# Kernel optimization log

Hardware: AMD Instinct MI355X
Metric: run time of the kernel (lower is better)

The kernel has to match this reference:

```python
import jax, jax.numpy as jnp
import numpy as np
import math

NB_HEADS = 16
NUM_BUCKETS = 32
MAX_DISTANCE = 128


def _rel_bucket(qlen, klen, num_buckets=NUM_BUCKETS, max_distance=MAX_DISTANCE):
    # static (numpy) computation of T5 relative-position buckets, bidirectional
    relpos = np.arange(qlen)[:, None] - np.arange(klen)[None, :]
    n = -relpos
    nb = num_buckets // 2
    ret = (n < 0).astype(np.int64) * nb
    n = np.abs(n)
    max_exact = nb // 2
    is_small = n < max_exact
    val_if_large = max_exact + (
        np.log(np.maximum(n, 1) / max_exact) / math.log(max_distance / max_exact) * (nb - max_exact)
    ).astype(np.int64)
    val_if_large = np.minimum(val_if_large, nb - 1)
    return ret + np.where(is_small, n, val_if_large)


def _layer_normalize(x):
    # faithful to source: mean/biased-std over last dim, NO epsilon, no affine
    m = jnp.mean(x, axis=-1, keepdims=True)
    var = jnp.mean((x - m) ** 2, axis=-1, keepdims=True)
    return (x - m) / jnp.sqrt(var)


def setup_inputs() -> dict:
    key = jax.random.key(0)
    ks = jax.random.split(key, 16)
    B, L, D, F = 4, 1024, 1024, 4096
    s = 0.02
    inp = {
        "x": jax.random.normal(ks[0], (B, L, D), jnp.float32),
        "padding_mask": jnp.ones((B, L), jnp.int32),
        "Wq": jax.random.normal(ks[1], (D, D), jnp.float32) * s,
        "bq": jnp.zeros((D,), jnp.float32),
        "Wk": jax.random.normal(ks[2], (D, D), jnp.float32) * s,
        "bk": jnp.zeros((D,), jnp.float32),
        "Wv": jax.random.normal(ks[3], (D, D), jnp.float32) * s,
        "bv": jnp.zeros((D,), jnp.float32),
        "Wo": jax.random.normal(ks[4], (D, D), jnp.float32) * s,
        "bo": jnp.zeros((D,), jnp.float32),
        "rel_emb": jax.random.normal(ks[5], (NUM_BUCKETS, NB_HEADS), jnp.float32) * s,
        "W1": jax.random.normal(ks[6], (F, D), jnp.float32) * s,
        "b1": jnp.zeros((F,), jnp.float32),
        "W2": jax.random.normal(ks[7], (D, F), jnp.float32) * s,
        "b2": jnp.zeros((D,), jnp.float32),
    }
    return inp


def reference(x, padding_mask, Wq, bq, Wk, bk, Wv, bv, Wo, bo, rel_emb, W1, b1, W2, b2):
    B, L, D = x.shape
    H = NB_HEADS
    dh = D // H

    q = x @ Wq.T + bq
    k = x @ Wk.T + bk
    v = x @ Wv.T + bv

    # NOTE: source does a RAW reshape (B, L, H*dh) -> (B*H, L, dh); reproduce exactly
    qm = q.reshape(B * H, L, dh)
    km = k.reshape(B * H, L, dh)
    vm = v.reshape(B * H, L, dh)

    scores = jnp.einsum("bqd,bkd->bqk", qm, km)  # (B*H, L, L), no 1/sqrt(dh) scaling in source

    # relative position bias: emb[bucket] -> (L, L, H), tile heads B times, permute
    buckets = jnp.asarray(_rel_bucket(L, L))
    pos = rel_emb[buckets]                      # (L, L, H)
    bias = jnp.transpose(jnp.tile(pos, (1, 1, B)), (2, 0, 1))  # (H*B, L, L)
    scores = scores + bias

    # padding mask in log space, tiled exactly like source's repeat+view
    pm = jnp.log(padding_mask.astype(jnp.float32))            # (B, L)
    mask = jnp.tile(pm[:, None, :], (1, L, H)).reshape(-1, L, L)  # (B*H, L, L)
    scores = scores + mask

    p = jax.nn.softmax(scores, axis=-1)  # dropout is identity at p=0 / eval
    att = (p @ vm).reshape(B, L, D)
    att = att @ Wo.T + bo

    att_out = _layer_normalize(att + x)
    ff = jax.nn.relu(att_out @ W1.T + b1) @ W2.T + b2
    ff_out = _layer_normalize(ff + att_out)
    return ff_out
```

## Files before the change

### kernel.cpp

```cpp
#include <hip/hip_runtime.h>
#include <hip/hip_bf16.h>

typedef __hip_bfloat16 bf16;
typedef __attribute__((ext_vector_type(8))) short s8v;
typedef __attribute__((ext_vector_type(4))) float f32x4;

__device__ __forceinline__ float bits2f(unsigned short u) {
    return __uint_as_float(((unsigned)u) << 16);
}
__device__ __forceinline__ unsigned short f2b(float f) {
    union { float f; unsigned u; } x{f};
    return (unsigned short)((x.u + 0x7fff + ((x.u >> 16) & 1)) >> 16);
}
__device__ __forceinline__ float to_f(float x) { return x; }
__device__ __forceinline__ float to_f(unsigned short x) { return bits2f(x); }

__device__ __forceinline__ void load4(const float* p, float* a) {
    float4 t = *(const float4*)p;
    a[0] = t.x; a[1] = t.y; a[2] = t.z; a[3] = t.w;
}
__device__ __forceinline__ void load4(const unsigned short* p, float* a) {
    ushort4 t = *(const ushort4*)p;
    a[0] = bits2f(t.x); a[1] = bits2f(t.y); a[2] = bits2f(t.z); a[3] = bits2f(t.w);
}

__global__ __launch_bounds__(256)
void cvt_all_kernel(const float* __restrict__ x,
                    const float* __restrict__ Wq, const float* __restrict__ Wk,
                    const float* __restrict__ Wv, const float* __restrict__ Wo,
                    const float* __restrict__ W1, const float* __restrict__ W2,
                    unsigned short* __restrict__ xb, unsigned short* __restrict__ Wqkvb,
                    unsigned short* __restrict__ Wob,
                    unsigned short* __restrict__ W1b, unsigned short* __restrict__ W2b)
{
    int i = blockIdx.x * 256 + threadIdx.x;
    const float* src; unsigned short* dst; int off;
    if (i < (1 << 20))      { src = x;  dst = xb;  off = i; }
    else if (i < (2 << 20)) { src = W1; dst = W1b; off = i - (1 << 20); }
    else if (i < (3 << 20)) { src = W2; dst = W2b; off = i - (2 << 20); }
    else {
        int j = i - (3 << 20);
        int sel = j >> 18;
        off = j & ((1 << 18) - 1);
        src = sel == 0 ? Wq : sel == 1 ? Wk : sel == 2 ? Wv : Wo;
        dst = sel == 3 ? Wob : Wqkvb + ((size_t)sel << 20);
    }
    float4 v = ((const float4*)src)[off];
    ushort4 o = { f2b(v.x), f2b(v.y), f2b(v.z), f2b(v.w) };
    ((ushort4*)dst)[off] = o;
}

__global__ void rbias_kernel(const float* __restrict__ rel_emb, unsigned short* __restrict__ rbias)
{
    int idx = blockIdx.x * 256 + threadIdx.x;
    if (idx >= 16 * 2048) return;
    int h = idx >> 11, q = idx & 2047;
    int n = q - 1023, ret = 0;
    if (n < 0) { ret = 16; n = -n; }
    int b;
    if (n < 8) b = n;
    else {
        double t = log((double)n / 8.0) / log(16.0) * 8.0;
        int v = 8 + (int)t;
        b = v < 15 ? v : 15;
    }
    rbias[idx] = f2b(rel_emb[(ret + b) * 16 + h]);
}

template<typename TC, typename TR, int RELU, int QKV>
__global__ __launch_bounds__(256)
void mfma_gemm(const unsigned short* __restrict__ A, int lda,
               const unsigned short* __restrict__ W, int ldw,
               const float* __restrict__ b0, const float* __restrict__ b1,
               const float* __restrict__ b2,
               const TR* __restrict__ res,
               void* __restrict__ C0, void* __restrict__ C1, void* __restrict__ C2,
               int ldc, int M, int N, int Ksplit)
{
    __shared__ unsigned short sm[4 * 128 * 32];
    const int tid = threadIdx.x;
    const int w = tid >> 6, lane = tid & 63;
    const int quad = lane >> 4, col = lane & 15;

    const int bid = blockIdx.x + gridDim.x * blockIdx.y;
    const int nwg = gridDim.x * gridDim.y;
    const int swz = (bid & 7) * (nwg >> 3) + (bid >> 3);
    const int m0 = (swz / gridDim.x) * 128;
    const int n0 = (swz % gridDim.x) * 128;

    const int wrow = (w & 1) * 64, wcol = (w >> 1) * 64;
    const int kz = blockIdx.z * Ksplit;
    const int NT = Ksplit >> 5;

    int sr0, sq0, sr1, sq1;
    {
        const int i0_ = tid;
        int sp = i0_ & 63, rl = ((sp >> 2) ^ (sp >> 4)) & 1;
        sr0 = ((i0_ >> 6) << 4) | ((sp >> 2) & 0xE) | rl;
        sq0 = (sp & 3) ^ ((((sp >> 3) & 1) << 1) | rl);
        const int i1_ = 256 + tid;
        sp = i1_ & 63; rl = ((sp >> 2) ^ (sp >> 4)) & 1;
        sr1 = ((i1_ >> 6) << 4) | ((sp >> 2) & 0xE) | rl;
        sq1 = (sp & 3) ^ ((((sp >> 3) & 1) << 1) | rl);
    }
    const unsigned off0 = (unsigned)__builtin_amdgcn_readfirstlane((unsigned)((0 * 256 + (tid & 192)) * 16));
    const unsigned off1 = (unsigned)__builtin_amdgcn_readfirstlane((unsigned)((1 * 256 + (tid & 192)) * 16));

#define STAGE32(buf, k0)                                                                     \
    {                                                                                        \
        unsigned short* As_ = sm + (buf) * 4096;                                             \
        unsigned short* Ws_ = sm + 8192 + (buf) * 4096;                                      \
        const unsigned short* ga0 = A + (size_t)(m0 + sr0) * lda + (k0) + sq0 * 8;           \
        __builtin_amdgcn_global_load_lds(                                                    \
            (const __attribute__((address_space(1))) unsigned int*)ga0,                      \
            (__attribute__((address_space(3))) unsigned int*)((char*)As_ + off0), 16, 0, 0); \
        const unsigned short* ga1 = A + (size_t)(m0 + sr1) * lda + (k0) + sq1 * 8;           \
        __builtin_amdgcn_global_load_lds(                                                    \
            (const __attribute__((address_space(1))) unsigned int*)ga1,                      \
            (__attribute__((address_space(3))) unsigned int*)((char*)As_ + off1), 16, 0, 0); \
        const unsigned short* gw0 = W + (size_t)(n0 + sr0) * ldw + (k0) + sq0 * 8;           \
        __builtin_amdgcn_global_load_lds(                                                    \
            (const __attribute__((address_space(1))) unsigned int*)gw0,                      \
            (__attribute__((address_space(3))) unsigned int*)((char*)Ws_ + off0), 16, 0, 0); \
        const unsigned short* gw1 = W + (size_t)(n0 + sr1) * ldw + (k0) + sq1 * 8;           \
        __builtin_amdgcn_global_load_lds(                                                    \
            (const __attribute__((address_space(1))) unsigned int*)gw1,                      \
            (__attribute__((address_space(3))) unsigned int*)((char*)Ws_ + off1), 16, 0, 0); \
    }

    f32x4 acc[4][4] = {};

    STAGE32(0, kz);

    for (int t = 0; t < NT; ++t) {
        __syncthreads();
        const int cur = t & 1;
        if (t + 1 < NT) STAGE32(cur ^ 1, kz + (t + 1) * 32);

        const unsigned short* As = sm + cur * 4096;
        const unsigned short* Ws = sm + 8192 + cur * 4096;
        s8v af[4], bfr[4];
        #pragma unroll
        for (int mt = 0; mt < 4; ++mt) {
            int rr = wrow + mt * 16 + col;
            af[mt] = *(const s8v*)(As + ((rr * 32 + ((quad ^ (rr & 3)) << 3)) ^ (((rr >> 2) & 1) << 5)));
        }
        #pragma unroll
        for (int nt = 0; nt < 4; ++nt) {
            int rr = wcol + nt * 16 + col;
            bfr[nt] = *(const s8v*)(Ws + ((rr * 32 + ((quad ^ (rr & 3)) << 3)) ^ (((rr >> 2) & 1) << 5)));
        }
        __builtin_amdgcn_s_setprio(1);
        #pragma unroll
        for (int mt = 0; mt < 4; ++mt)
            #pragma unroll
            for (int nt = 0; nt < 4; ++nt)
                acc[mt][nt] = __builtin_amdgcn_mfma_f32_16x16x32_bf16(af[mt], bfr[nt], acc[mt][nt], 0, 0, 0);
        __builtin_amdgcn_s_setprio(0);
    }
#undef STAGE32

    if (QKV) {
        const int sel = n0 >> 10;
        unsigned short* Cb = (unsigned short*)(sel == 0 ? C0 : sel == 1 ? C1 : C2);
        const float* bs = sel == 0 ? b0 : sel == 1 ? b1 : b2;
        #pragma unroll
        for (int mt = 0; mt < 4; ++mt)
            #pragma unroll
            for (int rg = 0; rg < 4; ++rg) {
                int gm = m0 + wrow + mt * 16 + quad * 4 + rg;
                #pragma unroll
                for (int nt = 0; nt < 4; ++nt) {
                    int gnc = (n0 + wcol + nt * 16 + col) & 1023;
                    Cb[(size_t)gm * 1024 + gnc] = f2b(acc[mt][nt][rg] + bs[gnc]);
                }
            }
    } else {
        void* Cv = blockIdx.z ? C1 : C0;
        const bool z0 = (blockIdx.z == 0);
        #pragma unroll
        for (int mt = 0; mt < 4; ++mt)
            #pragma unroll
            for (int rg = 0; rg < 4; ++rg) {
                int gm = m0 + wrow + mt * 16 + quad * 4 + rg;
                #pragma unroll
                for (int nt = 0; nt < 4; ++nt) {
                    int gn = n0 + wcol + nt * 16 + col;
                    float c = acc[mt][nt][rg];
                    if (z0) {
                        if (b0)  c += b0[gn];
                        if (res) c += to_f(res[(size_t)gm * ldc + gn]);
                    }
                    if (RELU) c = fmaxf(c, 0.f);
                    if (sizeof(TC) == 2) ((unsigned short*)Cv)[(size_t)gm * ldc + gn] = f2b(c);
                    else                 ((float*)Cv)[(size_t)gm * ldc + gn] = c;
                }
            }
    }
}

__global__ __launch_bounds__(256)
void vtrans_kernel(const unsigned short* __restrict__ v, unsigned short* __restrict__ vt)
{
    __shared__ unsigned short t[64][68];
    const int bpmm = blockIdx.x;
    const int bp = bpmm >> 6, mm = bpmm & 63;
    const unsigned short* vr = v + (size_t)(bp * 64 + mm) * 1024;
    const int tid = threadIdx.x;
    #pragma unroll
    for (int it = 0; it < 4; ++it) {
        int c = (tid >> 6) + it * 4;
        int d = tid & 63;
        t[d][c] = vr[c * 64 + d];
    }
    __syncthreads();
    int d = tid >> 2, qq = tid & 3;
    ushort4 o = { t[d][qq * 4 + 0], t[d][qq * 4 + 1], t[d][qq * 4 + 2], t[d][qq * 4 + 3] };
    *(ushort4*)(vt + (size_t)bp * 65536 + (size_t)d * 1024 + mm * 16 + qq * 4) = o;
}

__global__ __launch_bounds__(256, 2)
void attn_mfma_kernel(const unsigned short* __restrict__ qb,
                      const unsigned short* __restrict__ kb,
                      const unsigned short* __restrict__ vt,
                      const unsigned short* __restrict__ rbias,
                      const int* __restrict__ pmask,
                      unsigned short* __restrict__ att)
{
    __shared__ unsigned short Qs[128 * 64];
    __shared__ unsigned short KP[128 * 64];
    __shared__ unsigned short Vt[64 * 128];
    __shared__ unsigned short rbs[2048];
    __shared__ unsigned short pmls[1024];

    const int tid = threadIdx.x;
    const int w = tid >> 6, lane = tid & 63;
    const int quad = lane >> 4, col = lane & 15;
    const int bp = blockIdx.x, i0 = blockIdx.y * 128;
    const int h = bp & 15, bb = bp >> 4;
    const size_t base = (size_t)bp << 16;
    const int myrow0 = w * 32, myrow1 = w * 32 + 16;

    {
        const unsigned short* qg = qb + base + (size_t)i0 * 64;
        #pragma unroll
        for (int it = 0; it < 4; ++it) {
            int idx = it * 256 + tid;
            int r = idx >> 3, c = idx & 7;
            s8v d = *(const s8v*)(qg + (size_t)r * 64 + (c ^ (r & 7)) * 8);
            *(s8v*)(Qs + r * 64 + c * 8) = d;
        }
    }
    {
        const unsigned short* rg = rbias + h * 2048;
        #pragma unroll
        for (int it = 0; it < 8; ++it) rbs[it * 256 + tid] = rg[it * 256 + tid];
    }
    #pragma unroll
    for (int it = 0; it < 4; ++it) {
        int j = it * 256 + tid;
        pmls[j] = f2b(__logf((float)pmask[bb * 1024 + j]));
    }

    f32x4 O0[4] = {}, O1[4] = {};
    float lrow0[4] = {0.f, 0.f, 0.f, 0.f};
    float lrow1[4] = {0.f, 0.f, 0.f, 0.f};

    unsigned short* Pw = KP + w * 2048;

    for (int jt = 0; jt < 8; ++jt) {
        const int j0 = jt * 128;
        __syncthreads();
        {
            const unsigned short* kg = kb + base + (size_t)j0 * 64;
            #pragma unroll
            for (int it = 0; it < 4; ++it) {
                int idx = it * 256 + tid;
                int r = idx >> 3, c = idx & 7;
                s8v d = *(const s8v*)(kg + (size_t)r * 64 + (c ^ (r & 7)) * 8);
                *(s8v*)(KP + r * 64 + c * 8) = d;
            }
            const unsigned short* vg = vt + base + j0;
            #pragma unroll
            for (int it = 0; it < 4; ++it) {
                int idx = it * 256 + tid;
                int r = idx >> 4, c = idx & 15;
                s8v d = *(const s8v*)(vg + (size_t)r * 1024 + (c ^ (r & 15)) * 8);
                *(s8v*)(Vt + r * 128 + c * 8) = d;
            }
        }
        __syncthreads();

        f32x4 S0[8] = {}, S1[8] = {};
        #pragma unroll
        for (int ks = 0; ks < 2; ++ks) {
            int ar0 = myrow0 + col, ar1 = myrow1 + col;
            s8v a0 = *(const s8v*)(Qs + ar0 * 64 + (((ks * 4 + quad) ^ (ar0 & 7)) * 8));
            s8v a1 = *(const s8v*)(Qs + ar1 * 64 + (((ks * 4 + quad) ^ (ar1 & 7)) * 8));
            #pragma unroll
            for (int ct = 0; ct < 8; ++ct) {
                int br = ct * 16 + col;
                s8v b = *(const s8v*)(KP + br * 64 + (((ks * 4 + quad) ^ (br & 7)) * 8));
                S0[ct] = __builtin_amdgcn_mfma_f32_16x16x32_bf16(a0, b, S0[ct], 0, 0, 0);
                S1[ct] = __builtin_amdgcn_mfma_f32_16x16x32_bf16(a1, b, S1[ct], 0, 0, 0);
            }
        }

        #pragma unroll
        for (int ct = 0; ct < 8; ++ct) {
            int gj = j0 + ct * 16 + col;
            float pmv = bits2f(pmls[gj]);
            int d0 = gj - (i0 + myrow0 + quad * 4) + 1023;
            int d1 = gj - (i0 + myrow1 + quad * 4) + 1023;
            #pragma unroll
            for (int r = 0; r < 4; ++r) {
                float e0 = __expf(S0[ct][r] + bits2f(rbs[d0 - r]) + pmv);
                float e1 = __expf(S1[ct][r] + bits2f(rbs[d1 - r]) + pmv);
                S0[ct][r] = e0; lrow0[r] += e0;
                S1[ct][r] = e1; lrow1[r] += e1;
            }
        }

        __syncthreads();

        #pragma unroll
        for (int ct = 0; ct < 8; ++ct)
            #pragma unroll
            for (int r = 0; r < 4; ++r) {
                int lr = quad * 4 + r;
                int j = ct * 16 + col;
                Pw[lr * 128 + (((j >> 3) ^ lr) << 3) + (j & 7)] = f2b(S0[ct][r]);
            }
        #pragma unroll
        for (int kt = 0; kt < 4; ++kt) {
            int pr = col;
            s8v a = *(const s8v*)(Pw + pr * 128 + (((kt * 4 + quad) ^ pr) * 8));
            #pragma unroll
            for (int nt = 0; nt < 4; ++nt) {
                int vr = nt * 16 + col;
                s8v b = *(const s8v*)(Vt + vr * 128 + (((kt * 4 + quad) ^ (vr & 15)) * 8));
                O0[nt] = __builtin_amdgcn_mfma_f32_16x16x32_bf16(a, b, O0[nt], 0, 0, 0);
            }
        }

        #pragma unroll
        for (int ct = 0; ct < 8; ++ct)
            #pragma unroll
            for (int r = 0; r < 4; ++r) {
                int lr = quad * 4 + r;
                int j = ct * 16 + col;
                Pw[lr * 128 + (((j >> 3) ^ lr) << 3) + (j & 7)] = f2b(S1[ct][r]);
            }
        #pragma unroll
        for (int kt = 0; kt < 4; ++kt) {
            int pr = col;
            s8v a = *(const s8v*)(Pw + pr * 128 + (((kt * 4 + quad) ^ pr) * 8));
            #pragma unroll
            for (int nt = 0; nt < 4; ++nt) {
                int vr = nt * 16 + col;
                s8v b = *(const s8v*)(Vt + vr * 128 + (((kt * 4 + quad) ^ (vr & 15)) * 8));
                O1[nt] = __builtin_amdgcn_mfma_f32_16x16x32_bf16(a, b, O1[nt], 0, 0, 0);
            }
        }
    }

    #pragma unroll
    for (int off = 1; off < 16; off <<= 1)
        #pragma unroll
        for (int r = 0; r < 4; ++r) {
            lrow0[r] += __shfl_xor(lrow0[r], off);
            lrow1[r] += __shfl_xor(lrow1[r], off);
        }
    #pragma unroll
    for (int r = 0; r < 4; ++r) {
        lrow0[r] = 1.f / lrow0[r];
        lrow1[r] = 1.f / lrow1[r];
    }

    unsigned short* ag0 = att + base + (size_t)(i0 + myrow0) * 64;
    unsigned short* ag1 = att + base + (size_t)(i0 + myrow1) * 64;
    #pragma unroll
    for (int nt = 0; nt < 4; ++nt)
        #pragma unroll
        for (int r = 0; r < 4; ++r) {
            ag0[(size_t)(quad * 4 + r) * 64 + nt * 16 + col] = f2b(O0[nt][r] * lrow0[r]);
            ag1[(size_t)(quad * 4 + r) * 64 + nt * 16 + col] = f2b(O1[nt][r] * lrow1[r]);
        }
}

template<typename TIN>
__global__ __launch_bounds__(256)
void ln_kernel(const TIN* __restrict__ in1, const TIN* __restrict__ in2,
               float* __restrict__ outF, unsigned short* __restrict__ outB)
{
    __shared__ float sred[8];
    const int row = blockIdx.x;
    const int tid = threadIdx.x;
    const size_t off = (size_t)row * 1024 + tid * 4;
    float a[4];
    load4(in1 + off, a);
    if (in2) {
        float b[4];
        load4(in2 + off, b);
        #pragma unroll
        for (int i = 0; i < 4; ++i) a[i] += b[i];
    }

    float lsum = a[0] + a[1] + a[2] + a[3];
    #pragma unroll
    for (int o = 32; o; o >>= 1) lsum += __shfl_down(lsum, o);
    const int lane = tid & 63, wid = tid >> 6;
    if (lane == 0) sred[wid] = lsum;
    __syncthreads();
    if (tid == 0) sred[4] = (sred[0] + sred[1] + sred[2] + sred[3]) * (1.f / 1024.f);
    __syncthreads();
    const float mean = sred[4];

    float d0 = a[0] - mean, d1 = a[1] - mean, d2 = a[2] - mean, d3 = a[3] - mean;
    float lsq = d0 * d0 + d1 * d1 + d2 * d2 + d3 * d3;
    #pragma unroll
    for (int o = 32; o; o >>= 1) lsq += __shfl_down(lsq, o);
    __syncthreads();
    if (lane == 0) sred[wid] = lsq;
    __syncthreads();
    if (tid == 0) sred[5] = rsqrtf((sred[0] + sred[1] + sred[2] + sred[3]) * (1.f / 1024.f));
    __syncthreads();
    const float r = sred[5];

    float o0 = d0 * r, o1 = d1 * r, o2 = d2 * r, o3 = d3 * r;
    if (outF) {
        float4 o = {o0, o1, o2, o3};
        *(float4*)&outF[off] = o;
    }
    if (outB) {
        ushort4 o = { f2b(o0), f2b(o1), f2b(o2), f2b(o3) };
        *(ushort4*)&outB[off] = o;
    }
}

extern "C" void kernel_launch(void* const* d_in, const int* in_sizes, int n_in,
                              void* d_out, int out_size, void* d_ws, size_t ws_size,
                              hipStream_t stream)
{
    const float* x     = (const float*)d_in[0];
    const int*   pmask = (const int*)  d_in[1];
    const float* Wq    = (const float*)d_in[2];
    const float* bq    = (const float*)d_in[3];
    const float* Wk    = (const float*)d_in[4];
    const float* bk    = (const float*)d_in[5];
    const float* Wv    = (const float*)d_in[6];
    const float* bv    = (const float*)d_in[7];
    const float* Wo    = (const float*)d_in[8];
    const float* bo    = (const float*)d_in[9];
    const float* rel   = (const float*)d_in[10];
    const float* W1    = (const float*)d_in[11];
    const float* b1    = (const float*)d_in[12];
    const float* W2    = (const float*)d_in[13];
    const float* b2    = (const float*)d_in[14];

    const int M = 4096, D = 1024;
    dim3 blk(256);

    char* ws = (char*)d_ws;
    unsigned short* W1b   = (unsigned short*)(ws);
    unsigned short* W2b   = (unsigned short*)(ws + ( 8u << 20));
    unsigned short* xb    = (unsigned short*)(ws + (16u << 20));
    unsigned short* Wqkvb = (unsigned short*)(ws + (24u << 20));
    unsigned short* Wob   = (unsigned short*)(ws + (30u << 20));
    unsigned short* qb    = (unsigned short*)(ws + (32u << 20));
    unsigned short* kb    = (unsigned short*)(ws + (40u << 20));
    unsigned short* vb    = (unsigned short*)(ws + (48u << 20));
    unsigned short* vt    = (unsigned short*)(ws + (56u << 20));
    unsigned short* rbias = (unsigned short*)(ws + (64u << 20));
    float*          tmpA    = (float*)(ws + (32u << 20));
    float*          tmpB    = (float*)(ws + (48u << 20));
    unsigned short* attoutB = (unsigned short*)(ws + (16u << 20));
    unsigned short* ff1     = (unsigned short*)(ws + (32u << 20));
    unsigned short* ff2a    = (unsigned short*)(ws);
    unsigned short* ff2b    = (unsigned short*)(ws + (24u << 20));
    unsigned short* attb    = (unsigned short*)d_out;

    cvt_all_kernel<<<16384, blk, 0, stream>>>(x, Wq, Wk, Wv, Wo, W1, W2,
                                              xb, Wqkvb, Wob, W1b, W2b);
    rbias_kernel<<<128, blk, 0, stream>>>(rel, rbias);

    mfma_gemm<unsigned short, float, 0, 1><<<dim3(24, 32), blk, 0, stream>>>(
        xb, D, Wqkvb, D, bq, bk, bv, (const float*)nullptr, qb, kb, vb, D, M, 3072, D);

    vtrans_kernel<<<4096, blk, 0, stream>>>(vb, vt);

    attn_mfma_kernel<<<dim3(64, 8), blk, 0, stream>>>(qb, kb, vt, rbias, pmask, attb);

    mfma_gemm<float, float, 0, 0><<<dim3(8, 32, 2), blk, 0, stream>>>(
        attb, D, Wob, D, bo, nullptr, nullptr, x, tmpA, tmpB, nullptr, D, M, D, 512);
    ln_kernel<float><<<4096, blk, 0, stream>>>(tmpA, tmpB, nullptr, attoutB);

    mfma_gemm<unsigned short, float, 1, 0><<<dim3(32, 32), blk, 0, stream>>>(
        attoutB, D, W1b, D, b1, nullptr, nullptr, (const float*)nullptr,
        ff1, nullptr, nullptr, 4096, M, 4096, D);
    mfma_gemm<unsigned short, unsigned short, 0, 0><<<dim3(8, 32, 2), blk, 0, stream>>>(
        ff1, 4096, W2b, 4096, b2, nullptr, nullptr, attoutB, ff2a, ff2b, nullptr, D, M, D, 2048);
    ln_kernel<unsigned short><<<4096, blk, 0, stream>>>(ff2a, ff2b, (float*)d_out, nullptr);
}
```

Baseline: 408.3 us.

## Enlarge GEMM tile to 256x128 with 512-thread blocks and XCD-aware mapping

The GEMM kernel now uses 512 threads (8 waves) per block and computes a 256x128 output tile instead of 128x128, so each staged W tile is shared by twice as many rows. Block-to-tile mapping is replaced with an XCD-aware layout that splits rows and columns across the eight XCDs to improve L2 locality. The goal is fewer global loads per MFMA and better cache reuse. In exchange, LDS use per block rises and the grid has half as many blocks, which may reduce occupancy or leave the machine under-filled, especially for the split-K launches.

```diff
diff --git a/kernel.cpp b/kernel.cpp
--- a/kernel.cpp
+++ b/kernel.cpp
@@ -68,7 +68,7 @@
 }
 
 template<typename TC, typename TR, int RELU, int QKV>
-__global__ __launch_bounds__(256)
+__global__ __launch_bounds__(512)
 void mfma_gemm(const unsigned short* __restrict__ A, int lda,
                const unsigned short* __restrict__ W, int ldw,
                const float* __restrict__ b0, const float* __restrict__ b1,
@@ -77,68 +77,66 @@
                void* __restrict__ C0, void* __restrict__ C1, void* __restrict__ C2,
                int ldc, int M, int N, int Ksplit)
 {
-    __shared__ unsigned short sm[4 * 128 * 32];
+    __shared__ unsigned short sm[2 * 8192 + 2 * 4096];
     const int tid = threadIdx.x;
     const int w = tid >> 6, lane = tid & 63;
     const int quad = lane >> 4, col = lane & 15;
 
     const int bid = blockIdx.x + gridDim.x * blockIdx.y;
-    const int nwg = gridDim.x * gridDim.y;
-    const int swz = (bid & 7) * (nwg >> 3) + (bid >> 3);
-    const int m0 = (swz / gridDim.x) * 128;
-    const int n0 = (swz % gridDim.x) * 128;
-
-    const int wrow = (w & 1) * 64, wcol = (w >> 1) * 64;
+    const int xcd = bid & 7, j = bid >> 3;
+    const int rh = gridDim.y >> 1, cw = gridDim.x >> 2;
+    const int m0 = (((xcd & 1) * rh) + (j % rh)) * 256;
+    const int n0 = (((xcd >> 1) * cw) + (j / rh)) * 128;
+
+    const int wrow = (w & 3) * 64, wcol = (w >> 2) * 64;
     const int kz = blockIdx.z * Ksplit;
     const int NT = Ksplit >> 5;
 
-    int sr0, sq0, sr1, sq1;
+    int sr0, sq0, sr1, sq1, sr2, sq2;
     {
-        const int i0_ = tid;
-        int sp = i0_ & 63, rl = ((sp >> 2) ^ (sp >> 4)) & 1;
-        sr0 = ((i0_ >> 6) << 4) | ((sp >> 2) & 0xE) | rl;
+        int idx = tid;
+        int sp = idx & 63, rl = ((sp >> 2) ^ (sp >> 4)) & 1;
+        sr0 = ((idx >> 6) << 4) | ((sp >> 2) & 0xE) | rl;
         sq0 = (sp & 3) ^ ((((sp >> 3) & 1) << 1) | rl);
-        const int i1_ = 256 + tid;
-        sp = i1_ & 63; rl = ((sp >> 2) ^ (sp >> 4)) & 1;
-        sr1 = ((i1_ >> 6) << 4) | ((sp >> 2) & 0xE) | rl;
+        idx = 512 + tid;
+        sp = idx & 63; rl = ((sp >> 2) ^ (sp >> 4)) & 1;
+        sr1 = ((idx >> 6) << 4) | ((sp >> 2) & 0xE) | rl;
         sq1 = (sp & 3) ^ ((((sp >> 3) & 1) << 1) | rl);
-    }
-    const unsigned off0 = (unsigned)__builtin_amdgcn_readfirstlane((unsigned)((0 * 256 + (tid & 192)) * 16));
-    const unsigned off1 = (unsigned)__builtin_amdgcn_readfirstlane((unsigned)((1 * 256 + (tid & 192)) * 16));
-
-#define STAGE32(buf, k0)                                                                     \
+        sr2 = sr0; sq2 = sq0;
+    }
+    const unsigned offA0 = (unsigned)__builtin_amdgcn_readfirstlane((unsigned)((tid & 448) * 16));
+    const unsigned offA1 = (unsigned)__builtin_amdgcn_readfirstlane((unsigned)((512 + (tid & 448)) * 16));
+    const unsigned offW0 = offA0;
+
+#define STAGE(buf, k0)                                                                       \
     {                                                                                        \
-        unsigned short* As_ = sm + (buf) * 4096;                                             \
-        unsigned short* Ws_ = sm + 8192 + (buf) * 4096;                                      \
+        unsigned short* As_ = sm + (buf) * 8192;                                             \
+        unsigned short* Ws_ = sm + 16384 + (buf) * 4096;                                     \
         const unsigned short* ga0 = A + (size_t)(m0 + sr0) * lda + (k0) + sq0 * 8;           \
         __builtin_amdgcn_global_load_lds(                                                    \
             (const __attribute__((address_space(1))) unsigned int*)ga0,                      \
-            (__attribute__((address_space(3))) unsigned int*)((char*)As_ + off0), 16, 0, 0); \
+            (__attribute__((address_space(3))) unsigned int*)((char*)As_ + offA0), 16, 0, 0);\
         const unsigned short* ga1 = A + (size_t)(m0 + sr1) * lda + (k0) + sq1 * 8;           \
         __builtin_amdgcn_global_load_lds(                                                    \
             (const __attribute__((address_space(1))) unsigned int*)ga1,                      \
-            (__attribute__((address_space(3))) unsigned int*)((char*)As_ + off1), 16, 0, 0); \
-        const unsigned short* gw0 = W + (size_t)(n0 + sr0) * ldw + (k0) + sq0 * 8;           \
+            (__attribute__((address_space(3))) unsigned int*)((char*)As_ + offA1), 16, 0, 0);\
+        const unsigned short* gw0 = W + (size_t)(n0 + sr2) * ldw + (k0) + sq2 * 8;           \
         __builtin_amdgcn_global_load_lds(                                                    \
             (const __attribute__((address_space(1))) unsigned int*)gw0,                      \
-            (__attribute__((address_space(3))) unsigned int*)((char*)Ws_ + off0), 16, 0, 0); \
-        const unsigned short* gw1 = W + (size_t)(n0 + sr1) * ldw + (k0) + sq1 * 8;           \
-        __builtin_amdgcn_global_load_lds(                                                    \
-            (const __attribute__((address_space(1))) unsigned int*)gw1,                      \
-            (__attribute__((address_space(3))) unsigned int*)((char*)Ws_ + off1), 16, 0, 0); \
+            (__attribute__((address_space(3))) unsigned int*)((char*)Ws_ + offW0), 16, 0, 0);\
     }
 
     f32x4 acc[4][4] = {};
 
-    STAGE32(0, kz);
+    STAGE(0, kz);
 
     for (int t = 0; t < NT; ++t) {
         __syncthreads();
         const int cur = t & 1;
-        if (t + 1 < NT) STAGE32(cur ^ 1, kz + (t + 1) * 32);
-
-        const unsigned short* As = sm + cur * 4096;
-        const unsigned short* Ws = sm + 8192 + cur * 4096;
+        if (t + 1 < NT) STAGE(cur ^ 1, kz + (t + 1) * 32);
+
+        const unsigned short* As = sm + cur * 8192;
+        const unsigned short* Ws = sm + 16384 + cur * 4096;
         s8v af[4], bfr[4];
         #pragma unroll
         for (int mt = 0; mt < 4; ++mt) {
@@ -158,7 +156,7 @@
                 acc[mt][nt] = __builtin_amdgcn_mfma_f32_16x16x32_bf16(af[mt], bfr[nt], acc[mt][nt], 0, 0, 0);
         __builtin_amdgcn_s_setprio(0);
     }
-#undef STAGE32
+#undef STAGE
 
     if (QKV) {
         const int sel = n0 >> 10;
@@ -460,6 +458,7 @@
 
     const int M = 4096, D = 1024;
     dim3 blk(256);
+    dim3 gblk(512);
 
     char* ws = (char*)d_ws;
     unsigned short* W1b   = (unsigned short*)(ws);
@@ -484,21 +483,21 @@
                                               xb, Wqkvb, Wob, W1b, W2b);
     rbias_kernel<<<128, blk, 0, stream>>>(rel, rbias);
 
-    mfma_gemm<unsigned short, float, 0, 1><<<dim3(24, 32), blk, 0, stream>>>(
+    mfma_gemm<unsigned short, float, 0, 1><<<dim3(24, 16), gblk, 0, stream>>>(
         xb, D, Wqkvb, D, bq, bk, bv, (const float*)nullptr, qb, kb, vb, D, M, 3072, D);
 
     vtrans_kernel<<<4096, blk, 0, stream>>>(vb, vt);
 
     attn_mfma_kernel<<<dim3(64, 8), blk, 0, stream>>>(qb, kb, vt, rbias, pmask, attb);
 
-    mfma_gemm<float, float, 0, 0><<<dim3(8, 32, 2), blk, 0, stream>>>(
+    mfma_gemm<float, float, 0, 0><<<dim3(8, 16, 2), gblk, 0, stream>>>(
         attb, D, Wob, D, bo, nullptr, nullptr, x, tmpA, tmpB, nullptr, D, M, D, 512);
     ln_kernel<float><<<4096, blk, 0, stream>>>(tmpA, tmpB, nullptr, attoutB);
 
-    mfma_gemm<unsigned short, float, 1, 0><<<dim3(32, 32), blk, 0, stream>>>(
+    mfma_gemm<unsigned short, float, 1, 0><<<dim3(32, 16), gblk, 0, stream>>>(
         attoutB, D, W1b, D, b1, nullptr, nullptr, (const float*)nullptr,
         ff1, nullptr, nullptr, 4096, M, 4096, D);
-    mfma_gemm<unsigned short, unsigned short, 0, 0><<<dim3(8, 32, 2), blk, 0, stream>>>(
+    mfma_gemm<unsigned short, unsigned short, 0, 0><<<dim3(8, 16, 2), gblk, 0, stream>>>(
         ff1, 4096, W2b, 4096, b2, nullptr, nullptr, attoutB, ff2a, ff2b, nullptr, D, M, D, 2048);
     ln_kernel<unsigned short><<<4096, blk, 0, stream>>>(ff2a, ff2b, (float*)d_out, nullptr);
 }
```

After: 396.2 us. 1.03x faster.

## Add 256x128 tile GEMM with 512 threads for the FFN up-projection

Applied to the files above, without the earlier changes.

Adds a second MFMA GEMM variant that computes a 256x128 output tile per workgroup with 8 waves, and uses it for the W1 (FFN up-projection, ReLU) GEMM. Each workgroup reuses every staged W tile across twice as many A rows. A new block-to-tile mapping spreads contiguous M/N regions across the XCDs. The other GEMMs keep the 128x128 kernel. The larger tile uses more LDS per block and halves the number of blocks, which could lower occupancy and load balance.

```diff
diff --git a/kernel.cpp b/kernel.cpp
--- a/kernel.cpp
+++ b/kernel.cpp
@@ -69,13 +69,13 @@
 
 template<typename TC, typename TR, int RELU, int QKV>
 __global__ __launch_bounds__(256)
-void mfma_gemm(const unsigned short* __restrict__ A, int lda,
-               const unsigned short* __restrict__ W, int ldw,
-               const float* __restrict__ b0, const float* __restrict__ b1,
-               const float* __restrict__ b2,
-               const TR* __restrict__ res,
-               void* __restrict__ C0, void* __restrict__ C1, void* __restrict__ C2,
-               int ldc, int M, int N, int Ksplit)
+void mfma_gemm128(const unsigned short* __restrict__ A, int lda,
+                  const unsigned short* __restrict__ W, int ldw,
+                  const float* __restrict__ b0, const float* __restrict__ b1,
+                  const float* __restrict__ b2,
+                  const TR* __restrict__ res,
+                  void* __restrict__ C0, void* __restrict__ C1, void* __restrict__ C2,
+                  int ldc, int M, int N, int Ksplit)
 {
     __shared__ unsigned short sm[4 * 128 * 32];
     const int tid = threadIdx.x;
@@ -199,6 +199,136 @@
     }
 }
 
+template<typename TC, typename TR, int RELU, int QKV>
+__global__ __launch_bounds__(512)
+void mfma_gemm256(const unsigned short* __restrict__ A, int lda,
+                  const unsigned short* __restrict__ W, int ldw,
+                  const float* __restrict__ b0, const float* __restrict__ b1,
+                  const float* __restrict__ b2,
+                  const TR* __restrict__ res,
+                  void* __restrict__ C0, void* __restrict__ C1, void* __restrict__ C2,
+                  int ldc, int M, int N, int Ksplit)
+{
+    __shared__ unsigned short sm[2 * 8192 + 2 * 4096];
+    const int tid = threadIdx.x;
+    const int w = tid >> 6, lane = tid & 63;
+    const int quad = lane >> 4, col = lane & 15;
+
+    const int bid = blockIdx.x + gridDim.x * blockIdx.y;
+    const int xcd = bid & 7, j = bid >> 3;
+    const int rh = gridDim.y >> 1, cw = gridDim.x >> 2;
+    const int m0 = (((xcd & 1) * rh) + (j % rh)) * 256;
+    const int n0 = (((xcd >> 1) * cw) + (j / rh)) * 128;
+
+    const int wrow = (w & 3) * 64, wcol = (w >> 2) * 64;
+    const int kz = blockIdx.z * Ksplit;
+    const int NT = Ksplit >> 5;
+
+    int sr0, sq0, sr1, sq1, sr2, sq2;
+    {
+        int idx = tid;
+        int sp = idx & 63, rl = ((sp >> 2) ^ (sp >> 4)) & 1;
+        sr0 = ((idx >> 6) << 4) | ((sp >> 2) & 0xE) | rl;
+        sq0 = (sp & 3) ^ ((((sp >> 3) & 1) << 1) | rl);
+        idx = 512 + tid;
+        sp = idx & 63; rl = ((sp >> 2) ^ (sp >> 4)) & 1;
+        sr1 = ((idx >> 6) << 4) | ((sp >> 2) & 0xE) | rl;
+        sq1 = (sp & 3) ^ ((((sp >> 3) & 1) << 1) | rl);
+        sr2 = sr0; sq2 = sq0;
+    }
+    const unsigned offA0 = (unsigned)__builtin_amdgcn_readfirstlane((unsigned)((tid & 448) * 16));
+    const unsigned offA1 = (unsigned)__builtin_amdgcn_readfirstlane((unsigned)((512 + (tid & 448)) * 16));
+    const unsigned offW0 = offA0;
+
+#define STAGE(buf, k0)                                                                       \
+    {                                                                                        \
+        unsigned short* As_ = sm + (buf) * 8192;                                             \
+        unsigned short* Ws_ = sm + 16384 + (buf) * 4096;                                     \
+        const unsigned short* ga0 = A + (size_t)(m0 + sr0) * lda + (k0) + sq0 * 8;           \
+        __builtin_amdgcn_global_load_lds(                                                    \
+            (const __attribute__((address_space(1))) unsigned int*)ga0,                      \
+            (__attribute__((address_space(3))) unsigned int*)((char*)As_ + offA0), 16, 0, 0);\
+        const unsigned short* ga1 = A + (size_t)(m0 + sr1) * lda + (k0) + sq1 * 8;           \
+        __builtin_amdgcn_global_load_lds(                                                    \
+            (const __attribute__((address_space(1))) unsigned int*)ga1,                      \
+            (__attribute__((address_space(3))) unsigned int*)((char*)As_ + offA1), 16, 0, 0);\
+        const unsigned short* gw0 = W + (size_t)(n0 + sr2) * ldw + (k0) + sq2 * 8;           \
+        __builtin_amdgcn_global_load_lds(                                                    \
+            (const __attribute__((address_space(1))) unsigned int*)gw0,                      \
+            (__attribute__((address_space(3))) unsigned int*)((char*)Ws_ + offW0), 16, 0, 0);\
+    }
+
+    f32x4 acc[4][4] = {};
+
+    STAGE(0, kz);
+
+    for (int t = 0; t < NT; ++t) {
+        __syncthreads();
+        const int cur = t & 1;
+        if (t + 1 < NT) STAGE(cur ^ 1, kz + (t + 1) * 32);
+
+        const unsigned short* As = sm + cur * 8192;
+        const unsigned short* Ws = sm + 16384 + cur * 4096;
+        s8v af[4], bfr[4];
+        #pragma unroll
+        for (int mt = 0; mt < 4; ++mt) {
+            int rr = wrow + mt * 16 + col;
+            af[mt] = *(const s8v*)(As + ((rr * 32 + ((quad ^ (rr & 3)) << 3)) ^ (((rr >> 2) & 1) << 5)));
+        }
+        #pragma unroll
+        for (int nt = 0; nt < 4; ++nt) {
+            int rr = wcol + nt * 16 + col;
+            bfr[nt] = *(const s8v*)(Ws + ((rr * 32 + ((quad ^ (rr & 3)) << 3)) ^ (((rr >> 2) & 1) << 5)));
+        }
+        __builtin_amdgcn_s_setprio(1);
+        #pragma unroll
+        for (int mt = 0; mt < 4; ++mt)
+            #pragma unroll
+            for (int nt = 0; nt < 4; ++nt)
+                acc[mt][nt] = __builtin_amdgcn_mfma_f32_16x16x32_bf16(af[mt], bfr[nt], acc[mt][nt], 0, 0, 0);
+        __builtin_amdgcn_s_setprio(0);
+    }
+#undef STAGE
+
+    if (QKV) {
+        const int sel = n0 >> 10;
+        unsigned short* Cb = (unsigned short*)(sel == 0 ? C0 : sel == 1 ? C1 : C2);
+        const float* bs = sel == 0 ? b0 : sel == 1 ? b1 : b2;
+        #pragma unroll
+        for (int mt = 0; mt < 4; ++mt)
+            #pragma unroll
+            for (int rg = 0; rg < 4; ++rg) {
+                int gm = m0 + wrow + mt * 16 + quad * 4 + rg;
+                #pragma unroll
+                for (int nt = 0; nt < 4; ++nt) {
+                    int gnc = (n0 + wcol + nt * 16 + col) & 1023;
+                    Cb[(size_t)gm * 1024 + gnc] = f2b(acc[mt][nt][rg] + bs[gnc]);
+                }
+            }
+    } else {
+        void* Cv = blockIdx.z ? C1 : C0;
+        const bool z0 = (blockIdx.z == 0);
+        #pragma unroll
+        for (int mt = 0; mt < 4; ++mt)
+            #pragma unroll
+            for (int rg = 0; rg < 4; ++rg) {
+                int gm = m0 + wrow + mt * 16 + quad * 4 + rg;
+                #pragma unroll
+                for (int nt = 0; nt < 4; ++nt) {
+                    int gn = n0 + wcol + nt * 16 + col;
+                    float c = acc[mt][nt][rg];
+                    if (z0) {
+                        if (b0)  c += b0[gn];
+                        if (res) c += to_f(res[(size_t)gm * ldc + gn]);
+                    }
+                    if (RELU) c = fmaxf(c, 0.f);
+                    if (sizeof(TC) == 2) ((unsigned short*)Cv)[(size_t)gm * ldc + gn] = f2b(c);
+                    else                 ((float*)Cv)[(size_t)gm * ldc + gn] = c;
+                }
+            }
+    }
+}
+
 __global__ __launch_bounds__(256)
 void vtrans_kernel(const unsigned short* __restrict__ v, unsigned short* __restrict__ vt)
 {
@@ -460,6 +590,7 @@
 
     const int M = 4096, D = 1024;
     dim3 blk(256);
+    dim3 gblk(512);
 
     char* ws = (char*)d_ws;
     unsigned short* W1b   = (unsigned short*)(ws);
@@ -484,21 +615,21 @@
                                               xb, Wqkvb, Wob, W1b, W2b);
     rbias_kernel<<<128, blk, 0, stream>>>(rel, rbias);
 
-    mfma_gemm<unsigned short, float, 0, 1><<<dim3(24, 32), blk, 0, stream>>>(
+    mfma_gemm128<unsigned short, float, 0, 1><<<dim3(24, 32), blk, 0, stream>>>(
         xb, D, Wqkvb, D, bq, bk, bv, (const float*)nullptr, qb, kb, vb, D, M, 3072, D);
 
     vtrans_kernel<<<4096, blk, 0, stream>>>(vb, vt);
 
     attn_mfma_kernel<<<dim3(64, 8), blk, 0, stream>>>(qb, kb, vt, rbias, pmask, attb);
 
-    mfma_gemm<float, float, 0, 0><<<dim3(8, 32, 2), blk, 0, stream>>>(
+    mfma_gemm128<float, float, 0, 0><<<dim3(8, 32, 2), blk, 0, stream>>>(
         attb, D, Wob, D, bo, nullptr, nullptr, x, tmpA, tmpB, nullptr, D, M, D, 512);
     ln_kernel<float><<<4096, blk, 0, stream>>>(tmpA, tmpB, nullptr, attoutB);
 
-    mfma_gemm<unsigned short, float, 1, 0><<<dim3(32, 32), blk, 0, stream>>>(
+    mfma_gemm256<unsigned short, float, 1, 0><<<dim3(32, 16), gblk, 0, stream>>>(
         attoutB, D, W1b, D, b1, nullptr, nullptr, (const float*)nullptr,
         ff1, nullptr, nullptr, 4096, M, 4096, D);
-    mfma_gemm<unsigned short, unsigned short, 0, 0><<<dim3(8, 32, 2), blk, 0, stream>>>(
+    mfma_gemm128<unsigned short, unsigned short, 0, 0><<<dim3(8, 32, 2), blk, 0, stream>>>(
         ff1, 4096, W2b, 4096, b2, nullptr, nullptr, attoutB, ff2a, ff2b, nullptr, D, M, D, 2048);
     ln_kernel<unsigned short><<<4096, blk, 0, stream>>>(ff2a, ff2b, (float*)d_out, nullptr);
 }
```

New measurement: 383.4 us. 1.06x faster.
